# Optimization experiments

Measured on AMD Instinct MI355X. Metric: run time of the kernel, lower is better.

Reference implementation:

```python
import jax, jax.numpy as jnp
import numpy as np

VOCAB, EMBED, EN_H, DE_H, ATTN, LAYERS = 50000, 256, 512, 512, 256, 2
SEQ, BATCH = 1024, 64

def setup_inputs() -> dict:
    key = jax.random.key(0)
    ks = jax.random.split(key, 20)
    n = lambda k, shp: jax.random.normal(k, shp, dtype=jnp.float32)
    inp = {
        "cur_input": jax.random.randint(ks[0], (BATCH,), 0, VOCAB, dtype=jnp.int64) if jax.config.jax_enable_x64 else jax.random.randint(ks[0], (BATCH,), 0, VOCAB, dtype=jnp.int32),
        "h0": n(ks[1], (LAYERS, BATCH, DE_H)),
        "c0": n(ks[2], (LAYERS, BATCH, DE_H)),
        "enc_states": n(ks[3], (SEQ, BATCH, EN_H)),
        "attention_mask": jnp.ones((BATCH, SEQ), dtype=jnp.float32),
        # parameters
        "emb_table": n(ks[4], (VOCAB, EMBED)) * 0.02,
        "attn_W": n(ks[5], (EN_H + DE_H, ATTN)) * 0.02,   # attention_model: Linear(en+de, attn, bias=False)
        "attn_v": n(ks[6], (ATTN,)) * 0.02,               # Linear(attn, 1, bias=False)
        "cg_W": n(ks[7], (DE_H + EMBED + EN_H, EN_H)) * 0.02,  # context gate
        "cg_b": jnp.zeros((EN_H,), dtype=jnp.float32),
        "Wih0": n(ks[8], (4 * DE_H, EN_H + EMBED)) * 0.02,
        "Whh0": n(ks[9], (4 * DE_H, DE_H)) * 0.02,
        "bih0": jnp.zeros((4 * DE_H,), dtype=jnp.float32),
        "bhh0": jnp.zeros((4 * DE_H,), dtype=jnp.float32),
        "Wih1": n(ks[10], (4 * DE_H, DE_H)) * 0.02,
        "Whh1": n(ks[11], (4 * DE_H, DE_H)) * 0.02,
        "bih1": jnp.zeros((4 * DE_H,), dtype=jnp.float32),
        "bhh1": jnp.zeros((4 * DE_H,), dtype=jnp.float32),
        "out_W": n(ks[12], (DE_H, VOCAB)) * 0.02,
        "out_b": jnp.zeros((VOCAB,), dtype=jnp.float32),
    }
    return inp

def _lstm_cell(x, h, c, Wih, Whh, bih, bhh):
    gates = x @ Wih.T + h @ Whh.T + bih + bhh  # (B, 4H), torch gate order i,f,g,o
    i, f, g, o = jnp.split(gates, 4, axis=-1)
    c_new = jax.nn.sigmoid(f) * c + jax.nn.sigmoid(i) * jnp.tanh(g)
    h_new = jax.nn.sigmoid(o) * jnp.tanh(c_new)
    return h_new, c_new

def reference(cur_input, h0, c0, enc_states, attention_mask,
              emb_table, attn_W, attn_v, cg_W, cg_b,
              Wih0, Whh0, bih0, bhh0, Wih1, Whh1, bih1, bhh1,
              out_W, out_b):
    S, B, _ = enc_states.shape
    dec = h0[-1]  # (B, DE_H)
    # Bahdanau attention: score over seq dim
    dec_b = jnp.broadcast_to(dec[None], (S, B, dec.shape[-1]))
    feat = jnp.tanh(jnp.concatenate([enc_states, dec_b], axis=-1) @ attn_W)  # (S,B,ATTN)
    e = feat @ attn_v  # (S,B)
    e = jnp.where(attention_mask.T > 0, e, jnp.float32(-1e9))
    alpha = jax.nn.softmax(e, axis=0)  # (S,B)
    ctx = jnp.einsum('sb,sbh->bh', alpha, enc_states)  # (B, EN_H)
    # embedding + context gate
    emb = emb_table[cur_input]  # (B, EMBED)
    gate = jax.nn.sigmoid(jnp.concatenate([dec, emb, ctx], axis=-1) @ cg_W + cg_b)
    ctx = gate * ctx
    x = jnp.concatenate([emb, ctx], axis=-1)  # (B, EMBED+EN_H)
    # two-layer single-step LSTM
    h1, c1 = _lstm_cell(x, h0[0], c0[0], Wih0, Whh0, bih0, bhh0)
    h2, c2 = _lstm_cell(h1, h0[1], c0[1], Wih1, Whh1, bih1, bhh1)
    out = h2 @ out_W + out_b  # (B, VOCAB)
    return out, jnp.stack([h1, h2]), jnp.stack([c1, c2])
```

## Files before the change

### kernel.cpp

```cpp
#include <hip/hip_runtime.h>
#include <math.h>


typedef __attribute__((ext_vector_type(8))) short short8;
typedef __attribute__((ext_vector_type(4))) float f32x4;

__device__ __forceinline__ float sigf(float x) { return 1.f / (1.f + expf(-x)); }

__device__ __forceinline__ unsigned short f2bf(float f) {
    unsigned int u = __builtin_bit_cast(unsigned int, f);
    unsigned int r = (u + 0x7fffu + ((u >> 16) & 1u)) >> 16;
    return (unsigned short)r;
}

__device__ __forceinline__ unsigned cvt_pk(float lo, float hi) {
    unsigned r;
    asm("v_cvt_pk_bf16_f32 %0, %1, %2" : "=v"(r) : "v"(lo), "v"(hi));
    return r;
}

__device__ __forceinline__ float tanh_fast(float x) {
    float t = __expf(2.f * x);
    return 1.f - 2.f * __builtin_amdgcn_rcpf(1.f + t);
}

__global__ void k_prep_conv(const int* __restrict__ cur, const float* __restrict__ h0,
                            const float* __restrict__ emb_table, const float* __restrict__ attn_W,
                            float* __restrict__ X1, float* __restrict__ X2, float* __restrict__ X3,
                            float* __restrict__ decW, unsigned short* __restrict__ Wt) {
    int t = threadIdx.x;
    if (blockIdx.x >= 64) {
        __shared__ float tile[64][65];
        int bx = blockIdx.x - 64;
        int kb = (bx & 7) * 64, nb = (bx >> 3) * 64;
        int r0 = t >> 6, c = t & 63;
#pragma unroll
        for (int i = 0; i < 16; ++i) {
            int r = i * 4 + r0;
            tile[r][c] = attn_W[(size_t)(kb + r) * 256 + nb + c];
        }
        __syncthreads();
#pragma unroll
        for (int i = 0; i < 16; ++i) {
            int r = i * 4 + r0;
            int n = nb + r;
            int byte = ((n * 128 + ((c >> 3) << 4)) ^ ((r & 7) << 4)) + ((c & 7) << 1);
            *(unsigned short*)((char*)Wt + kb * 512 + byte) = f2bf(tile[c][r]);
        }
        return;
    }
    __shared__ float dec_s[512];
    int b = blockIdx.x;
    const float* dec = h0 + (size_t)(64 + b) * 512;
    for (int i = t; i < 512; i += 256) {
        float v = dec[i];
        dec_s[i] = v;
        X1[b * 1280 + i] = v;
        X2[b * 1280 + 768 + i] = h0[(size_t)b * 512 + i];
        X3[b * 1024 + 512 + i] = v;
    }
    int row = cur[b];
    float ev = emb_table[(size_t)row * 256 + t];
    X1[b * 1280 + 512 + t] = ev;
    X2[b * 1280 + t] = ev;
    __syncthreads();
    float acc = 0.f;
    for (int k = 0; k < 512; ++k)
        acc += dec_s[k] * attn_W[(size_t)(512 + k) * 256 + t];
    decW[b * 256 + t] = acc;
}

__global__ __launch_bounds__(256) void k_scores_mfma(
        const float* __restrict__ enc, const unsigned short* __restrict__ Wt,
        const float* __restrict__ attn_v, const float* __restrict__ decW,
        float* __restrict__ e_out) {
    int s = blockIdx.x, t = threadIdx.x;
    __shared__ __align__(16) unsigned short sA[2][4096];
    __shared__ __align__(16) unsigned short sB[16384];
    const float* arow = enc + (size_t)s * 64 * 512;
    int w = t >> 6, l = t & 63, li = l & 15, lg = l >> 4;
    int sw = (li & 7) << 4;

    int ar0 = t >> 3, akg0 = t & 7;
    int ar1 = (256 + t) >> 3;
    int abyte0 = (ar0 * 128 + akg0 * 16) ^ ((ar0 & 7) << 4);
    int abyte1 = (ar1 * 128 + akg0 * 16) ^ ((ar1 & 7) << 4);
    int bbase = w * 8192 + l * 16;

    f32x4 acc[4][4];
#pragma unroll
    for (int rt = 0; rt < 4; ++rt)
#pragma unroll
        for (int ct = 0; ct < 4; ++ct) acc[rt][ct] = (f32x4){0.f, 0.f, 0.f, 0.f};

    float4 aP[4];
    uint4  bP[8];

#pragma unroll
    for (int i = 0; i < 2; ++i) {
        const float* g = arow + (ar0 + i * 32) * 512 + akg0 * 8;
        aP[2 * i] = *(const float4*)g;
        aP[2 * i + 1] = *(const float4*)(g + 4);
    }
#pragma unroll
    for (int j = 0; j < 8; ++j)
        bP[j] = *(const uint4*)((const char*)Wt + bbase + j * 1024);
    {
        uint4 wv0, wv1;
        wv0.x = cvt_pk(aP[0].x, aP[0].y); wv0.y = cvt_pk(aP[0].z, aP[0].w);
        wv0.z = cvt_pk(aP[1].x, aP[1].y); wv0.w = cvt_pk(aP[1].z, aP[1].w);
        wv1.x = cvt_pk(aP[2].x, aP[2].y); wv1.y = cvt_pk(aP[2].z, aP[2].w);
        wv1.z = cvt_pk(aP[3].x, aP[3].y); wv1.w = cvt_pk(aP[3].z, aP[3].w);
        *(uint4*)((char*)sA[0] + abyte0) = wv0;
        *(uint4*)((char*)sA[0] + abyte1) = wv1;
#pragma unroll
        for (int j = 0; j < 8; ++j)
            *(uint4*)((char*)sB + bbase + j * 1024) = bP[j];
    }
    __syncthreads();

    for (int kk = 0; kk < 8; ++kk) {
        int cur = kk & 1;
        if (kk < 7) {
            int ko = (kk + 1) * 64;
#pragma unroll
            for (int i = 0; i < 2; ++i) {
                const float* g = arow + (ar0 + i * 32) * 512 + ko + akg0 * 8;
                aP[2 * i] = *(const float4*)g;
                aP[2 * i + 1] = *(const float4*)(g + 4);
            }
            const char* src = (const char*)Wt + ((kk + 1) << 15);
#pragma unroll
            for (int j = 0; j < 8; ++j)
                bP[j] = *(const uint4*)(src + bbase + j * 1024);
        }
#pragma unroll
        for (int ks = 0; ks < 2; ++ks) {
            short8 af[4], bf[4];
#pragma unroll
            for (int rt = 0; rt < 4; ++rt) {
                int row = rt * 16 + li;
                af[rt] = *(short8*)((char*)sA[cur] + ((row * 128 + ks * 64 + lg * 16) ^ sw));
            }
#pragma unroll
            for (int ct = 0; ct < 4; ++ct) {
                int n = w * 64 + ct * 16 + li;
                bf[ct] = *(short8*)((char*)sB + ((n * 128 + ks * 64 + lg * 16) ^ sw));
            }
#pragma unroll
            for (int rt = 0; rt < 4; ++rt)
#pragma unroll
                for (int ct = 0; ct < 4; ++ct)
                    acc[rt][ct] = __builtin_amdgcn_mfma_f32_16x16x32_bf16(
                        af[rt], bf[ct], acc[rt][ct], 0, 0, 0);
        }
        if (kk < 7) {
            uint4 wv0, wv1;
            wv0.x = cvt_pk(aP[0].x, aP[0].y); wv0.y = cvt_pk(aP[0].z, aP[0].w);
            wv0.z = cvt_pk(aP[1].x, aP[1].y); wv0.w = cvt_pk(aP[1].z, aP[1].w);
            wv1.x = cvt_pk(aP[2].x, aP[2].y); wv1.y = cvt_pk(aP[2].z, aP[2].w);
            wv1.z = cvt_pk(aP[3].x, aP[3].y); wv1.w = cvt_pk(aP[3].z, aP[3].w);
            *(uint4*)((char*)sA[cur ^ 1] + abyte0) = wv0;
            *(uint4*)((char*)sA[cur ^ 1] + abyte1) = wv1;
#pragma unroll
            for (int j = 0; j < 8; ++j)
                *(uint4*)((char*)sB + bbase + j * 1024) = bP[j];
        }
        __syncthreads();
    }

    float er[4][4];
#pragma unroll
    for (int rt = 0; rt < 4; ++rt)
#pragma unroll
        for (int r = 0; r < 4; ++r) er[rt][r] = 0.f;
#pragma unroll
    for (int ct = 0; ct < 4; ++ct) {
        int a = w * 64 + ct * 16 + li;
        float v = attn_v[a];
#pragma unroll
        for (int rt = 0; rt < 4; ++rt) {
#pragma unroll
            for (int r = 0; r < 4; ++r) {
                int row = rt * 16 + lg * 4 + r;
                float x = acc[rt][ct][r] + decW[row * 256 + a];
                er[rt][r] += tanh_fast(x) * v;
            }
        }
    }
#pragma unroll
    for (int off = 1; off < 16; off <<= 1)
#pragma unroll
        for (int rt = 0; rt < 4; ++rt)
#pragma unroll
            for (int r = 0; r < 4; ++r)
                er[rt][r] += __shfl_xor(er[rt][r], off, 64);
    float* part = (float*)sA[0];
    if (li == 0) {
#pragma unroll
        for (int rt = 0; rt < 4; ++rt)
#pragma unroll
            for (int r = 0; r < 4; ++r)
                part[w * 64 + rt * 16 + lg * 4 + r] = er[rt][r];
    }
    __syncthreads();
    if (t < 64)
        e_out[t * 1024 + s] = part[t] + part[64 + t] + part[128 + t] + part[192 + t];
}

__global__ __launch_bounds__(512) void k_ctx_partial(const float* __restrict__ ebuf,
        const float* __restrict__ mask, const float* __restrict__ enc,
        float* __restrict__ ctxP) {
    int b = blockIdx.x & 63, sc = blockIdx.x >> 6;
    int t = threadIdx.x;
    __shared__ float al[128];
    __shared__ float red[16];
    float v0 = ebuf[b * 1024 + t];
    float v1 = ebuf[b * 1024 + 512 + t];
    v0 = (mask[b * 1024 + t] > 0.f) ? v0 : -1e9f;
    v1 = (mask[b * 1024 + 512 + t] > 0.f) ? v1 : -1e9f;
    float lmax = fmaxf(v0, v1);
#pragma unroll
    for (int off = 32; off > 0; off >>= 1) lmax = fmaxf(lmax, __shfl_xor(lmax, off, 64));
    if ((t & 63) == 0) red[t >> 6] = lmax;
    __syncthreads();
    float m = red[0];
#pragma unroll
    for (int i = 1; i < 8; ++i) m = fmaxf(m, red[i]);
    float lsum = __expf(v0 - m) + __expf(v1 - m);
#pragma unroll
    for (int off = 32; off > 0; off >>= 1) lsum += __shfl_xor(lsum, off, 64);
    if ((t & 63) == 0) red[8 + (t >> 6)] = lsum;
    __syncthreads();
    float tot = red[8];
#pragma unroll
    for (int i = 1; i < 8; ++i) tot += red[8 + i];
    float inv = 1.f / tot;
    if (t < 128) {
        int s = sc * 128 + t;
        float x = ebuf[b * 1024 + s];
        x = (mask[b * 1024 + s] > 0.f) ? x : -1e9f;
        al[t] = __expf(x - m) * inv;
    }
    __syncthreads();
    const float* base = enc + (((size_t)sc * 128 * 64) + b) * 512 + t;
    float a0 = 0.f, a1 = 0.f, a2 = 0.f, a3 = 0.f;
    for (int s = 0; s < 128; s += 4) {
        float x0 = base[(size_t)(s + 0) * 32768];
        float x1 = base[(size_t)(s + 1) * 32768];
        float x2 = base[(size_t)(s + 2) * 32768];
        float x3 = base[(size_t)(s + 3) * 32768];
        a0 += al[s] * x0; a1 += al[s + 1] * x1; a2 += al[s + 2] * x2; a3 += al[s + 3] * x3;
    }
    ctxP[((size_t)sc * 64 + b) * 512 + t] = a0 + a1 + a2 + a3;
}

__global__ __launch_bounds__(1024) void k_gemm_cg(const float* __restrict__ X,
        const float* __restrict__ ctxP, const float* __restrict__ Wkn,
        float* __restrict__ P) {
    int n0 = blockIdx.x * 64, sp = blockIdx.y;
    int t = threadIdx.x, tc = t & 63, tr = t >> 6;
    __shared__ __align__(16) float As[64 * 68];
    __shared__ __align__(16) float Wc[64 * 68];
    float acc[4] = {0.f, 0.f, 0.f, 0.f};
    for (int c = 0; c < 5; ++c) {
        int k0 = sp * 320 + c * 64;
        __syncthreads();
#pragma unroll
        for (int i = 0; i < 4; ++i) {
            int idx = i * 1024 + t; int row = idx >> 6; int k = idx & 63;
            int gk = k0 + k;
            float v;
            if (gk < 768) {
                v = X[row * 1280 + gk];
            } else {
                int h = gk - 768;
                v = 0.f;
#pragma unroll
                for (int sc = 0; sc < 8; ++sc)
                    v += ctxP[((size_t)sc * 64 + row) * 512 + h];
            }
            As[k * 68 + row] = v;
        }
#pragma unroll
        for (int i = 0; i < 4; ++i) {
            int idx = i * 1024 + t; int k = idx >> 6; int cc = idx & 63;
            Wc[k * 68 + cc] = Wkn[(size_t)(k0 + k) * 512 + n0 + cc];
        }
        __syncthreads();
#pragma unroll 8
        for (int k = 0; k < 64; ++k) {
            float4 a = *(const float4*)&As[k * 68 + 4 * tr];
            float wv = Wc[k * 68 + tc];
            acc[0] += a.x * wv; acc[1] += a.y * wv; acc[2] += a.z * wv; acc[3] += a.w * wv;
        }
    }
    float* Pp = P + (size_t)sp * 32768;
#pragma unroll
    for (int j = 0; j < 4; ++j) Pp[(4 * tr + j) * 512 + n0 + tc] = acc[j];
}

__global__ void k_cg_fin(const float* __restrict__ P, const float* __restrict__ cg_b,
                         const float* __restrict__ ctxP, float* __restrict__ X2) {
    int idx = blockIdx.x * 256 + threadIdx.x;
    int b = idx >> 9, h = idx & 511;
    float g = cg_b[h];
#pragma unroll
    for (int sp = 0; sp < 4; ++sp) g += P[sp * 32768 + idx];
    float ctx = 0.f;
#pragma unroll
    for (int sc = 0; sc < 8; ++sc) ctx += ctxP[((size_t)sc * 64 + b) * 512 + h];
    X2[b * 1280 + 256 + h] = sigf(g) * ctx;
}

__global__ __launch_bounds__(1024) void k_gemm_lstm(const float* __restrict__ X, int ldx,
        const float* __restrict__ W1, int K1, const float* __restrict__ W2, int K2,
        int kchunks, float* __restrict__ P) {
    int n0 = blockIdx.x * 64, sp = blockIdx.y;
    int t = threadIdx.x, tc = t & 63, tr = t >> 6;
    __shared__ __align__(16) float As[64 * 68];
    __shared__ __align__(16) float Wc[64 * 68];
    float acc[4] = {0.f, 0.f, 0.f, 0.f};
    for (int c = 0; c < kchunks; ++c) {
        int k0 = (sp * kchunks + c) * 64;
        __syncthreads();
#pragma unroll
        for (int i = 0; i < 4; ++i) {
            int idx = i * 1024 + t; int row = idx >> 6; int k = idx & 63;
            As[k * 68 + row] = X[row * ldx + k0 + k];
        }
#pragma unroll
        for (int i = 0; i < 4; ++i) {
            int idx = i * 1024 + t; int cc = idx >> 6; int k = idx & 63;
            int gk = k0 + k; int j = n0 + cc;
            float wv = (gk < K1) ? W1[(size_t)j * K1 + gk] : W2[(size_t)j * K2 + gk - K1];
            Wc[k * 68 + cc] = wv;
        }
        __syncthreads();
#pragma unroll 8
        for (int k = 0; k < 64; ++k) {
            float4 a = *(const float4*)&As[k * 68 + 4 * tr];
            float wv = Wc[k * 68 + tc];
            acc[0] += a.x * wv; acc[1] += a.y * wv; acc[2] += a.z * wv; acc[3] += a.w * wv;
        }
    }
    float* Pp = P + (size_t)sp * 64 * 2048;
#pragma unroll
    for (int j = 0; j < 4; ++j) Pp[(4 * tr + j) * 2048 + n0 + tc] = acc[j];
}

__global__ void k_lstm_fin(const float* __restrict__ P, const float* __restrict__ bih,
                           const float* __restrict__ bhh, const float* __restrict__ c0,
                           int layer, float* __restrict__ oh, float* __restrict__ oc,
                           float* __restrict__ X3out) {
    int idx = blockIdx.x * 256 + threadIdx.x;
    int b = idx >> 9, h = idx & 511;
    float gi = bih[h] + bhh[h];
    float gf = bih[512 + h] + bhh[512 + h];
    float gg = bih[1024 + h] + bhh[1024 + h];
    float go = bih[1536 + h] + bhh[1536 + h];
#pragma unroll
    for (int sp = 0; sp < 4; ++sp) {
        const float* Pp = P + sp * 131072 + b * 2048;
        gi += Pp[h]; gf += Pp[512 + h]; gg += Pp[1024 + h]; go += Pp[1536 + h];
    }
    float cp = c0[layer * 32768 + b * 512 + h];
    float cn = sigf(gf) * cp + sigf(gi) * tanhf(gg);
    float hn = sigf(go) * tanhf(cn);
    oh[b * 512 + h] = hn;
    oc[b * 512 + h] = cn;
    if (X3out) X3out[b * 1024 + h] = hn;
}

__global__ __launch_bounds__(256) void k_outproj_mfma(
        const float* __restrict__ h2, const float* __restrict__ out_W,
        const float* __restrict__ out_b, float* __restrict__ out) {
    int t = threadIdx.x;
    int n0 = blockIdx.x * 64;
    int w = t >> 6, l = t & 63, li = l & 15, lg = l >> 4;
    int sw = (li & 7) << 4;
    __shared__ __align__(16) unsigned short sA[16384];

    f32x4 acc[4];
#pragma unroll
    for (int rt = 0; rt < 4; ++rt) acc[rt] = (f32x4){0.f, 0.f, 0.f, 0.f};
    int col = n0 + w * 16 + li;
    int colc = (col < 50000) ? col : 49999;

    for (int ph = 0; ph < 2; ++ph) {
        __syncthreads();
#pragma unroll
        for (int i = 0; i < 8; ++i) {
            int idx = i * 256 + t;
            int row = idx >> 5, kg = idx & 31;
            const float* g = h2 + row * 512 + ph * 256 + kg * 8;
            float4 p0 = *(const float4*)g;
            float4 p1 = *(const float4*)(g + 4);
            uint4 wv;
            wv.x = cvt_pk(p0.x, p0.y); wv.y = cvt_pk(p0.z, p0.w);
            wv.z = cvt_pk(p1.x, p1.y); wv.w = cvt_pk(p1.z, p1.w);
            int byte = (row * 512 + kg * 16) ^ ((row & 7) << 4);
            *(uint4*)((char*)sA + byte) = wv;
        }
        __syncthreads();
#pragma unroll
        for (int cc = 0; cc < 4; ++cc) {
#pragma unroll
            for (int ks = 0; ks < 2; ++ks) {
                int kk = ph * 256 + cc * 64 + ks * 32;
                const float* wp = out_W + (size_t)(kk + lg * 8) * 50000 + colc;
                uint4 qv;
                float v0 = wp[0],          v1 = wp[50000];
                float v2 = wp[2 * 50000],  v3 = wp[3 * 50000];
                float v4 = wp[4 * 50000],  v5 = wp[5 * 50000];
                float v6 = wp[6 * 50000],  v7 = wp[7 * 50000];
                qv.x = cvt_pk(v0, v1); qv.y = cvt_pk(v2, v3);
                qv.z = cvt_pk(v4, v5); qv.w = cvt_pk(v6, v7);
                short8 bf = *(short8*)&qv;
                short8 af[4];
#pragma unroll
                for (int rt = 0; rt < 4; ++rt) {
                    int row = rt * 16 + li;
                    af[rt] = *(short8*)((char*)sA +
                        ((row * 512 + cc * 128 + ks * 64 + lg * 16) ^ sw));
                }
#pragma unroll
                for (int rt = 0; rt < 4; ++rt)
                    acc[rt] = __builtin_amdgcn_mfma_f32_16x16x32_bf16(
                        af[rt], bf, acc[rt], 0, 0, 0);
            }
        }
    }
    if (col < 50000) {
        float bias = out_b[col];
#pragma unroll
        for (int rt = 0; rt < 4; ++rt)
#pragma unroll
            for (int r = 0; r < 4; ++r) {
                int row = rt * 16 + lg * 4 + r;
                out[(size_t)row * 50000 + col] = acc[rt][r] + bias;
            }
    }
}

extern "C" void kernel_launch(void* const* d_in, const int* in_sizes, int n_in,
                              void* d_out, int out_size, void* d_ws, size_t ws_size,
                              hipStream_t stream) {
    const int*   cur       = (const int*)d_in[0];
    const float* h0        = (const float*)d_in[1];
    const float* c0        = (const float*)d_in[2];
    const float* enc       = (const float*)d_in[3];
    const float* mask      = (const float*)d_in[4];
    const float* emb_table = (const float*)d_in[5];
    const float* attn_W    = (const float*)d_in[6];
    const float* attn_v    = (const float*)d_in[7];
    const float* cg_W      = (const float*)d_in[8];
    const float* cg_b      = (const float*)d_in[9];
    const float* Wih0      = (const float*)d_in[10];
    const float* Whh0      = (const float*)d_in[11];
    const float* bih0      = (const float*)d_in[12];
    const float* bhh0      = (const float*)d_in[13];
    const float* Wih1      = (const float*)d_in[14];
    const float* Whh1      = (const float*)d_in[15];
    const float* bih1      = (const float*)d_in[16];
    const float* bhh1      = (const float*)d_in[17];
    const float* out_W     = (const float*)d_in[18];
    const float* out_b     = (const float*)d_in[19];
    float* out = (float*)d_out;

    float* w    = (float*)d_ws;
    float* X1   = w;
    float* X2   = X1 + 81920;
    float* X3   = X2 + 81920;
    float* decW = X3 + 65536;
    float* eb   = decW + 16384;
    float* P    = eb + 65536;
    float* ctxP = P + 524288;
    unsigned short* Wt = (unsigned short*)P;

    float* outH = out + 3200000;
    float* outC = out + 3265536;

    hipLaunchKernelGGL(k_prep_conv, dim3(96), dim3(256), 0, stream,
                       cur, h0, emb_table, attn_W, X1, X2, X3, decW, Wt);
    hipLaunchKernelGGL(k_scores_mfma, dim3(1024), dim3(256), 0, stream,
                       enc, Wt, attn_v, decW, eb);
    hipLaunchKernelGGL(k_ctx_partial, dim3(512), dim3(512), 0, stream,
                       eb, mask, enc, ctxP);
    hipLaunchKernelGGL(k_gemm_cg, dim3(8, 4), dim3(1024), 0, stream,
                       X1, ctxP, cg_W, P);
    hipLaunchKernelGGL(k_cg_fin, dim3(128), dim3(256), 0, stream, P, cg_b, ctxP, X2);
    hipLaunchKernelGGL(k_gemm_lstm, dim3(32, 4), dim3(1024), 0, stream,
                       X2, 1280, Wih0, 768, Whh0, 512, 5, P);
    hipLaunchKernelGGL(k_lstm_fin, dim3(128), dim3(256), 0, stream,
                       P, bih0, bhh0, c0, 0, outH, outC, X3);
    hipLaunchKernelGGL(k_gemm_lstm, dim3(32, 4), dim3(1024), 0, stream,
                       X3, 1024, Wih1, 512, Whh1, 512, 4, P);
    hipLaunchKernelGGL(k_lstm_fin, dim3(128), dim3(256), 0, stream,
                       P, bih1, bhh1, c0, 1, outH + 32768, outC + 32768, (float*)nullptr);
    hipLaunchKernelGGL(k_outproj_mfma, dim3(782), dim3(256), 0, stream,
                       outH + 32768, out_W, out_b, out);
}
```

Baseline: 196.1 us.

## Split output projection K dimension across two wave groups with LDS reduction

```diff
diff --git a/kernel.cpp b/kernel.cpp
--- a/kernel.cpp
+++ b/kernel.cpp
@@ -372,74 +372,81 @@
     if (X3out) X3out[b * 1024 + h] = hn;
 }
 
-__global__ __launch_bounds__(256) void k_outproj_mfma(
+__global__ __launch_bounds__(512) void k_outproj_mfma(
         const float* __restrict__ h2, const float* __restrict__ out_W,
         const float* __restrict__ out_b, float* __restrict__ out) {
     int t = threadIdx.x;
     int n0 = blockIdx.x * 64;
     int w = t >> 6, l = t & 63, li = l & 15, lg = l >> 4;
     int sw = (li & 7) << 4;
-    __shared__ __align__(16) unsigned short sA[16384];
+    int wc = w & 3, kh = w >> 2;
+    __shared__ __align__(16) unsigned short sA[2][4096];
 
     f32x4 acc[4];
 #pragma unroll
     for (int rt = 0; rt < 4; ++rt) acc[rt] = (f32x4){0.f, 0.f, 0.f, 0.f};
-    int col = n0 + w * 16 + li;
+    int col = n0 + wc * 16 + li;
     int colc = (col < 50000) ? col : 49999;
 
-    for (int ph = 0; ph < 2; ++ph) {
-        __syncthreads();
-#pragma unroll
-        for (int i = 0; i < 8; ++i) {
-            int idx = i * 256 + t;
-            int row = idx >> 5, kg = idx & 31;
-            const float* g = h2 + row * 512 + ph * 256 + kg * 8;
+    int srow = t >> 3, skg = t & 7;
+    int abyte = (srow * 128 + skg * 16) ^ ((srow & 7) << 4);
+
+    for (int c = 0; c < 4; ++c) {
+        __syncthreads();
+#pragma unroll
+        for (int h = 0; h < 2; ++h) {
+            const float* g = h2 + srow * 512 + h * 256 + c * 64 + skg * 8;
             float4 p0 = *(const float4*)g;
             float4 p1 = *(const float4*)(g + 4);
             uint4 wv;
             wv.x = cvt_pk(p0.x, p0.y); wv.y = cvt_pk(p0.z, p0.w);
             wv.z = cvt_pk(p1.x, p1.y); wv.w = cvt_pk(p1.z, p1.w);
-            int byte = (row * 512 + kg * 16) ^ ((row & 7) << 4);
-            *(uint4*)((char*)sA + byte) = wv;
-        }
-        __syncthreads();
-#pragma unroll
-        for (int cc = 0; cc < 4; ++cc) {
-#pragma unroll
-            for (int ks = 0; ks < 2; ++ks) {
-                int kk = ph * 256 + cc * 64 + ks * 32;
-                const float* wp = out_W + (size_t)(kk + lg * 8) * 50000 + colc;
-                uint4 qv;
-                float v0 = wp[0],          v1 = wp[50000];
-                float v2 = wp[2 * 50000],  v3 = wp[3 * 50000];
-                float v4 = wp[4 * 50000],  v5 = wp[5 * 50000];
-                float v6 = wp[6 * 50000],  v7 = wp[7 * 50000];
-                qv.x = cvt_pk(v0, v1); qv.y = cvt_pk(v2, v3);
-                qv.z = cvt_pk(v4, v5); qv.w = cvt_pk(v6, v7);
-                short8 bf = *(short8*)&qv;
-                short8 af[4];
-#pragma unroll
-                for (int rt = 0; rt < 4; ++rt) {
-                    int row = rt * 16 + li;
-                    af[rt] = *(short8*)((char*)sA +
-                        ((row * 512 + cc * 128 + ks * 64 + lg * 16) ^ sw));
-                }
-#pragma unroll
-                for (int rt = 0; rt < 4; ++rt)
-                    acc[rt] = __builtin_amdgcn_mfma_f32_16x16x32_bf16(
-                        af[rt], bf, acc[rt], 0, 0, 0);
-            }
-        }
-    }
-    if (col < 50000) {
+            *(uint4*)((char*)sA[h] + abyte) = wv;
+        }
+        __syncthreads();
+#pragma unroll
+        for (int ks = 0; ks < 2; ++ks) {
+            int kk = kh * 256 + c * 64 + ks * 32;
+            const float* wp = out_W + (size_t)(kk + lg * 8) * 50000 + colc;
+            uint4 qv;
+            float v0 = wp[0],          v1 = wp[50000];
+            float v2 = wp[2 * 50000],  v3 = wp[3 * 50000];
+            float v4 = wp[4 * 50000],  v5 = wp[5 * 50000];
+            float v6 = wp[6 * 50000],  v7 = wp[7 * 50000];
+            qv.x = cvt_pk(v0, v1); qv.y = cvt_pk(v2, v3);
+            qv.z = cvt_pk(v4, v5); qv.w = cvt_pk(v6, v7);
+            short8 bf = *(short8*)&qv;
+            short8 af[4];
+#pragma unroll
+            for (int rt = 0; rt < 4; ++rt) {
+                int row = rt * 16 + li;
+                af[rt] = *(short8*)((char*)sA[kh] + ((row * 128 + ks * 64 + lg * 16) ^ sw));
+            }
+#pragma unroll
+            for (int rt = 0; rt < 4; ++rt)
+                acc[rt] = __builtin_amdgcn_mfma_f32_16x16x32_bf16(
+                    af[rt], bf, acc[rt], 0, 0, 0);
+        }
+    }
+    __syncthreads();
+    float* red = (float*)sA;
+    if (kh == 1) {
+#pragma unroll
+        for (int rt = 0; rt < 4; ++rt)
+            *(f32x4*)&red[wc * 1024 + rt * 256 + l * 4] = acc[rt];
+    }
+    __syncthreads();
+    if (kh == 0 && col < 50000) {
         float bias = out_b[col];
 #pragma unroll
-        for (int rt = 0; rt < 4; ++rt)
+        for (int rt = 0; rt < 4; ++rt) {
+            f32x4 o = *(f32x4*)&red[wc * 1024 + rt * 256 + l * 4];
 #pragma unroll
             for (int r = 0; r < 4; ++r) {
                 int row = rt * 16 + lg * 4 + r;
-                out[(size_t)row * 50000 + col] = acc[rt][r] + bias;
-            }
+                out[(size_t)row * 50000 + col] = acc[rt][r] + o[r] + bias;
+            }
+        }
     }
 }
 
@@ -498,6 +505,6 @@
                        X3, 1024, Wih1, 512, Whh1, 512, 4, P);
     hipLaunchKernelGGL(k_lstm_fin, dim3(128), dim3(256), 0, stream,
                        P, bih1, bhh1, c0, 1, outH + 32768, outC + 32768, (float*)nullptr);
-    hipLaunchKernelGGL(k_outproj_mfma, dim3(782), dim3(256), 0, stream,
+    hipLaunchKernelGGL(k_outproj_mfma, dim3(782), dim3(512), 0, stream,
                        outH + 32768, out_W, out_b, out);
 }
```

New measurement: 179.1 us, median of 2. 1.1x faster.
